# Performance work log

Measured on AMD Instinct MI355X. Metric: run time of the kernel, lower is better.

Reference implementation:

```python
import jax, jax.numpy as jnp
import numpy as np

D = 1  # dilation


def _unfold3x3(x, d):
    # x: [B, C, H, W] -> [B, H*W, 9, C]; matches torch.nn.Unfold(kernel_size=3,
    # dilation=d, padding=d, stride=1) followed by the module's reshapes.
    B, C, H, W = x.shape
    xp = jnp.pad(x, ((0, 0), (0, 0), (d, d), (d, d)))
    pats = [xp[:, :, i * d:i * d + H, j * d:j * d + W] for i in range(3) for j in range(3)]
    p = jnp.stack(pats, axis=0)  # [9, B, C, H, W], kernel positions row-major (center = 4)
    return p.transpose(1, 3, 4, 0, 2).reshape(B, H * W, 9, C)


def _masked_bn(h, m, gamma, beta, eps=1e-5):
    # BatchNorm1d in training mode applied only to rows selected by bool mask m
    # (the torch code gathers rows, BNs them, scatters back into zeros).
    # Stats are the biased mean/var over the selected rows, per channel.
    axes = tuple(range(h.ndim - 1))
    mf = m[..., None].astype(h.dtype)
    n = jnp.maximum(mf.sum(), 1.0)
    mean = (h * mf).sum(axes) / n
    var = (((h - mean) ** 2 * mf)).sum(axes) / n
    return (h - mean) * jax.lax.rsqrt(var + eps) * gamma + beta


def setup_inputs() -> dict:
    key = jax.random.key(0)
    ks = jax.random.split(key, 8)
    B, H, W = 2, 64, 1024
    Cin, Cout, Cm = 64, 64, 4
    s = 0.1
    x = jax.random.normal(ks[0], (B, Cm + Cin, H, W), jnp.float32)
    mask = (jax.random.uniform(ks[1], (B, 1, H, W)) > 0.3).astype(jnp.float32)
    return {
        "x": x,
        "mask": mask,
        "w1": jax.random.normal(ks[2], (8, Cm), jnp.float32) * s,
        "bn1_g": jnp.ones(8, jnp.float32),
        "bn1_b": jnp.zeros(8, jnp.float32),
        "w2": jax.random.normal(ks[3], (1, 8), jnp.float32) * s,
        "b2": jnp.zeros(1, jnp.float32),
        "g1": jax.random.normal(ks[4], (8, Cm), jnp.float32) * s,
        "gbn1_g": jnp.ones(8, jnp.float32),
        "gbn1_b": jnp.zeros(8, jnp.float32),
        "g2": jax.random.normal(ks[5], (8, 8), jnp.float32) * s,
        "gbn2_g": jnp.ones(8, jnp.float32),
        "gbn2_b": jnp.zeros(8, jnp.float32),
        "w_agg": jax.random.normal(ks[6], (Cout, 72 + Cin), jnp.float32) * s,
        "abn_g": jnp.ones(Cout, jnp.float32),
        "abn_b": jnp.zeros(Cout, jnp.float32),
    }


def reference(x, mask, w1, bn1_g, bn1_b, w2, b2, g1, gbn1_g, gbn1_b, g2, gbn2_g, gbn2_b, w_agg, abn_g, abn_b):
    B, C, H, W = x.shape
    xu = _unfold3x3(x, D)                      # [B, HW, 9, C]
    mu = _unfold3x3(mask, D)[..., 0]           # [B, HW, 9]
    msel = mu > 0                              # valid-neighbor mask
    mp0 = msel[:, :, 4]                        # valid-center mask [B, HW]
    pn = xu[..., :4] - xu[:, :, 4:5, :4]       # relative meta coords [B, HW, 9, 4]
    feats = xu[..., 4:]                        # neighbor features [B, HW, 9, Cin]

    # weight branch (dense compute + mask == torch's gather/scatter)
    h = _masked_bn(pn @ w1.T, msel, bn1_g, bn1_b)
    h = jax.nn.relu(h) @ w2.T + b2             # [B, HW, 9, 1]
    wts = jnp.where(msel, h[..., 0], 0.0)      # zeros at invalid neighbors pre-softmax
    wts = jax.nn.softmax(wts, axis=-1)[..., None]

    fagg = (wts * feats).sum(axis=2)           # [B, HW, Cin]

    # geo branch
    g = jax.nn.relu(_masked_bn(pn @ g1.T, msel, gbn1_g, gbn1_b))
    g = jax.nn.relu(_masked_bn(g @ g2.T, msel, gbn2_g, gbn2_b))
    g = jnp.where(msel[..., None], g, 0.0)
    g = (wts * g).reshape(B, H * W, 72)

    # aggregation over valid centers
    out = jnp.concatenate([fagg, g], axis=-1) @ w_agg.T
    out = jax.nn.relu(_masked_bn(out, mp0, abn_g, abn_b))
    out = jnp.where(mp0[..., None], out, 0.0)  # [B, HW, Cout]
    return out.transpose(0, 2, 1).reshape(B, -1, H, W)  # fold with k=1 == reshape
```

## Files before the change

kernel.cpp:

```cpp
#include <hip/hip_runtime.h>

#define HW_ 65536
#define W_ 1024
#define H_ 64
#define B_ 2
#define C_ 68
#define NPIX 131072
#define EPS 1e-5f
#define SCOLS 258
#define STOT (15 * SCOLS)

typedef __attribute__((ext_vector_type(8))) short short8;
typedef __attribute__((ext_vector_type(4))) float floatx4;

__device__ __forceinline__ unsigned short f2bf(float f) {
  unsigned u = __float_as_uint(f);
  u += 0x7fffu + ((u >> 16) & 1u);
  return (unsigned short)(u >> 16);
}
__device__ __forceinline__ unsigned pack2(float a, float b) {
  return (unsigned)f2bf(a) | ((unsigned)f2bf(b) << 16);
}
__device__ __forceinline__ float wred(float v) {
  v += __shfl_xor(v, 1);  v += __shfl_xor(v, 2);  v += __shfl_xor(v, 4);
  v += __shfl_xor(v, 8);  v += __shfl_xor(v, 16); v += __shfl_xor(v, 32);
  return v;
}
__device__ __forceinline__ int swz_tile(int bid) {
  return (bid & 7) * 64 + (bid >> 3);
}

#define XSTG(ch, row, col) stg[((ch) * 3 + (row)) * SCOLS + (col)]
#define MSTG(row, col)     stg[(12 + (row)) * SCOLS + (col)]

template <int NT>
__device__ __forceinline__ void stage_rows(const float* xb, const float* mb,
                                           int h, int w0, float* stg, int tid) {
#pragma unroll 1
  for (int i = tid; i < STOT; i += NT) {
    int seg = i / SCOLS, col = i - seg * SCOLS;
    int arr = seg / 3, row = seg - arr * 3;
    int wg = w0 - 1 + col, hg = h + row - 1;
    bool ok = ((unsigned)wg < (unsigned)W_) && ((unsigned)hg < (unsigned)H_);
    float v = 0.f;
    if (ok) v = (arr < 4) ? xb[(size_t)arr * HW_ + (hg << 10) + wg]
                          : mb[(hg << 10) + wg];
    stg[i] = v;
  }
}

__global__ __launch_bounds__(256, 4) void k_stats1(
    const float* __restrict__ x, const float* __restrict__ mask,
    float* __restrict__ ws) {
  __shared__ float stg[STOT];
  __shared__ float red[4][16];
  int tile = swz_tile(blockIdx.x);
  int p0 = tile * 256;
  int b = p0 >> 16, s0 = p0 & (HW_ - 1);
  int h = s0 >> 10, w0 = s0 & (W_ - 1);
  const float* xb = x + (size_t)b * C_ * HW_;
  const float* mb = mask + (size_t)b * HW_;
  stage_rows<256>(xb, mb, h, w0, stg, threadIdx.x);
  __syncthreads();

  int pix = threadIdx.x;
  float xc0 = XSTG(0, 1, 1 + pix), xc1 = XSTG(1, 1, 1 + pix);
  float xc2 = XSTG(2, 1, 1 + pix), xc3 = XSTG(3, 1, 1 + pix);

  float a[16];
#pragma unroll
  for (int i = 0; i < 16; i++) a[i] = 0.f;
  a[15] = (MSTG(1, 1 + pix) > 0.f) ? 1.f : 0.f;

#pragma unroll
  for (int k = 0; k < 9; k++) {
    int row = k / 3, col = 1 + pix + (k % 3 - 1);
    float mval = MSTG(row, col);
    if (mval > 0.f) {
      float pn0 = XSTG(0, row, col) - xc0;
      float pn1 = XSTG(1, row, col) - xc1;
      float pn2 = XSTG(2, row, col) - xc2;
      float pn3 = XSTG(3, row, col) - xc3;
      a[14] += 1.f;
      a[0] += pn0; a[1] += pn1; a[2] += pn2; a[3] += pn3;
      a[4] += pn0 * pn0; a[5] += pn0 * pn1; a[6] += pn0 * pn2; a[7] += pn0 * pn3;
      a[8] += pn1 * pn1; a[9] += pn1 * pn2; a[10] += pn1 * pn3;
      a[11] += pn2 * pn2; a[12] += pn2 * pn3; a[13] += pn3 * pn3;
    }
  }
  int lane = threadIdx.x & 63, wave = threadIdx.x >> 6;
#pragma unroll
  for (int i = 0; i < 16; i++) {
    float rv = wred(a[i]);
    if (lane == 0) red[wave][i] = rv;
  }
  __syncthreads();
  if (threadIdx.x < 16)
    atomicAdd(&ws[threadIdx.x],
              red[0][threadIdx.x] + red[1][threadIdx.x] + red[2][threadIdx.x] + red[3][threadIdx.x]);
}

__global__ __launch_bounds__(256, 4) void k_stats2(
    const float* __restrict__ x, const float* __restrict__ mask,
    const float* __restrict__ g1, const float* __restrict__ gbn1_g,
    const float* __restrict__ gbn1_b, const float* __restrict__ g2,
    float* __restrict__ ws) {
  __shared__ float stg[STOT];
  __shared__ float red[4][16];
  __shared__ float sc[8], sh[8];
  if (threadIdx.x < 8) {
    int o = threadIdx.x;
    float a0 = g1[o * 4], a1 = g1[o * 4 + 1], a2 = g1[o * 4 + 2], a3 = g1[o * 4 + 3];
    float n = fmaxf(ws[14], 1.f);
    float mean = (a0 * ws[0] + a1 * ws[1] + a2 * ws[2] + a3 * ws[3]) / n;
    float q = a0 * a0 * ws[4] + a1 * a1 * ws[8] + a2 * a2 * ws[11] + a3 * a3 * ws[13]
            + 2.f * (a0 * a1 * ws[5] + a0 * a2 * ws[6] + a0 * a3 * ws[7]
                   + a1 * a2 * ws[9] + a1 * a3 * ws[10] + a2 * a3 * ws[12]);
    float var = q / n - mean * mean;
    float s_ = gbn1_g[o] * rsqrtf(var + EPS);
    sc[o] = s_; sh[o] = gbn1_b[o] - mean * s_;
  }
  int half = blockIdx.x >> 9;
  int tile = swz_tile(blockIdx.x & 511);
  int p0 = tile * 256;
  int b = p0 >> 16, s0 = p0 & (HW_ - 1);
  int h = s0 >> 10, w0 = s0 & (W_ - 1);
  const float* xb = x + (size_t)b * C_ * HW_;
  const float* mb = mask + (size_t)b * HW_;
  stage_rows<256>(xb, mb, h, w0, stg, threadIdx.x);
  __syncthreads();

  int pix = threadIdx.x;
  float xc0 = XSTG(0, 1, 1 + pix), xc1 = XSTG(1, 1, 1 + pix);
  float xc2 = XSTG(2, 1, 1 + pix), xc3 = XSTG(3, 1, 1 + pix);

  float acc2[16];
#pragma unroll
  for (int i = 0; i < 16; i++) acc2[i] = 0.f;

  int kb = half ? 5 : 0, ke = half ? 9 : 5;
#pragma unroll
  for (int k = 0; k < 9; k++) {
    if (k < kb || k >= ke) continue;
    int row = k / 3, col = 1 + pix + (k % 3 - 1);
    float mval = MSTG(row, col);
    if (mval > 0.f) {
      float pn0 = XSTG(0, row, col) - xc0;
      float pn1 = XSTG(1, row, col) - xc1;
      float pn2 = XSTG(2, row, col) - xc2;
      float pn3 = XSTG(3, row, col) - xc3;
      float gb[8];
#pragma unroll
      for (int o = 0; o < 8; o++) {
        float tg = pn0 * g1[o * 4] + pn1 * g1[o * 4 + 1] + pn2 * g1[o * 4 + 2] + pn3 * g1[o * 4 + 3];
        gb[o] = fmaxf(sc[o] * tg + sh[o], 0.f);
      }
#pragma unroll
      for (int j = 0; j < 8; j++) {
        float t2 = 0.f;
#pragma unroll
        for (int o = 0; o < 8; o++) t2 += gb[o] * g2[j * 8 + o];
        acc2[j] += t2; acc2[8 + j] += t2 * t2;
      }
    }
  }
  int lane = threadIdx.x & 63, wave = threadIdx.x >> 6;
#pragma unroll
  for (int i = 0; i < 16; i++) {
    float rv = wred(acc2[i]);
    if (lane == 0) red[wave][i] = rv;
  }
  __syncthreads();
  if (threadIdx.x < 16)
    atomicAdd(&ws[40 + threadIdx.x],
              red[0][threadIdx.x] + red[1][threadIdx.x] + red[2][threadIdx.x] + red[3][threadIdx.x]);
}

__global__ __launch_bounds__(512, 4) void k_fused(
    const float* __restrict__ x, const float* __restrict__ mask,
    const float* __restrict__ w1, const float* __restrict__ bn1_g,
    const float* __restrict__ bn1_b, const float* __restrict__ w2,
    const float* __restrict__ b2, const float* __restrict__ g1,
    const float* __restrict__ gbn1_g, const float* __restrict__ gbn1_b,
    const float* __restrict__ g2, const float* __restrict__ gbn2_g,
    const float* __restrict__ gbn2_b, const float* __restrict__ w_agg,
    const float* __restrict__ ws, float* __restrict__ out_pre,
    float* __restrict__ wsum) {
  __shared__ uint4 vecA[17][256];
  __shared__ float evb[9][256];
  __shared__ float sA[8], hA[8], sG1[8], hG1[8], sG2[8], hG2[8];
  float* stg = (float*)&vecA[0][0];

  if (threadIdx.x < 16) {
    int o = threadIdx.x & 7;
    const float* wv = (threadIdx.x < 8) ? w1 : g1;
    float a0 = wv[o * 4], a1 = wv[o * 4 + 1], a2 = wv[o * 4 + 2], a3 = wv[o * 4 + 3];
    float n = fmaxf(ws[14], 1.f);
    float mean = (a0 * ws[0] + a1 * ws[1] + a2 * ws[2] + a3 * ws[3]) / n;
    float q = a0 * a0 * ws[4] + a1 * a1 * ws[8] + a2 * a2 * ws[11] + a3 * a3 * ws[13]
            + 2.f * (a0 * a1 * ws[5] + a0 * a2 * ws[6] + a0 * a3 * ws[7]
                   + a1 * a2 * ws[9] + a1 * a3 * ws[10] + a2 * a3 * ws[12]);
    float var = q / n - mean * mean;
    float gma = (threadIdx.x < 8) ? bn1_g[o] : gbn1_g[o];
    float bta = (threadIdx.x < 8) ? bn1_b[o] : gbn1_b[o];
    float s_ = gma * rsqrtf(var + EPS);
    float sft = bta - mean * s_;
    if (threadIdx.x < 8) { sA[o] = s_;  hA[o] = sft; }
    else                 { sG1[o] = s_; hG1[o] = sft; }
  } else if (threadIdx.x < 24) {
    int o = threadIdx.x & 7;
    float n = fmaxf(ws[14], 1.f);
    float mean = ws[40 + o] / n, var = ws[48 + o] / n - mean * mean;
    float s_ = gbn2_g[o] * rsqrtf(var + EPS);
    sG2[o] = s_; hG2[o] = gbn2_b[o] - mean * s_;
  }

  int tid = threadIdx.x;
  int half = tid >> 8;
  int pix = tid & 255;
  int tile = swz_tile(blockIdx.x);
  int p0 = tile * 256;
  int b = p0 >> 16, s0 = p0 & (HW_ - 1);
  int h = s0 >> 10, w0 = s0 & (W_ - 1);
  const float* xb = x + (size_t)b * C_ * HW_;
  const float* mb = mask + (size_t)b * HW_;
  stage_rows<512>(xb, mb, h, w0, stg, tid);
  __syncthreads();

  float xc0 = XSTG(0, 1, 1 + pix), xc1 = XSTG(1, 1, 1 + pix);
  float xc2 = XSTG(2, 1, 1 + pix), xc3 = XSTG(3, 1, 1 + pix);
  float b2v = b2[0];

  float pnc[5][4];
  unsigned mbits = 0u;
  int kb = half ? 5 : 0, ke = half ? 9 : 5;
#pragma unroll
  for (int k = 0; k < 9; k++) {
    if (k < kb || k >= ke) continue;
    int j = k - kb;
    int row = k / 3, col = 1 + pix + (k % 3 - 1);
    float mval = MSTG(row, col);
    float wp = 0.f;
    pnc[j][0] = 0.f; pnc[j][1] = 0.f; pnc[j][2] = 0.f; pnc[j][3] = 0.f;
    if (mval > 0.f) {
      mbits |= (1u << k);
      pnc[j][0] = XSTG(0, row, col) - xc0;
      pnc[j][1] = XSTG(1, row, col) - xc1;
      pnc[j][2] = XSTG(2, row, col) - xc2;
      pnc[j][3] = XSTG(3, row, col) - xc3;
      float accw = 0.f;
#pragma unroll
      for (int o = 0; o < 8; o++) {
        float ta = pnc[j][0] * w1[o * 4] + pnc[j][1] * w1[o * 4 + 1] +
                   pnc[j][2] * w1[o * 4 + 2] + pnc[j][3] * w1[o * 4 + 3];
        accw += fmaxf(sA[o] * ta + hA[o], 0.f) * w2[o];
      }
      wp = accw + b2v;
    }
    evb[k][pix] = wp;
  }
  __syncthreads();

  float ev[9];
  float mx = -1e30f;
#pragma unroll
  for (int k = 0; k < 9; k++) { ev[k] = evb[k][pix]; mx = fmaxf(mx, ev[k]); }
  float den = 0.f;
#pragma unroll
  for (int k = 0; k < 9; k++) { ev[k] = __expf(ev[k] - mx); den += ev[k]; }
  float inv = 1.f / den;

#pragma unroll
  for (int k = 0; k < 9; k++) {
    if (k < kb || k >= ke) continue;
    int j = k - kb;
    uint4 pk; pk.x = pk.y = pk.z = pk.w = 0u;
    if ((mbits >> k) & 1u) {
      float wt = ev[k] * inv;
      float gb[8];
#pragma unroll
      for (int o = 0; o < 8; o++) {
        float tg = pnc[j][0] * g1[o * 4] + pnc[j][1] * g1[o * 4 + 1] +
                   pnc[j][2] * g1[o * 4 + 2] + pnc[j][3] * g1[o * 4 + 3];
        gb[o] = fmaxf(sG1[o] * tg + hG1[o], 0.f);
      }
      float gv[8];
#pragma unroll
      for (int j2 = 0; j2 < 8; j2++) {
        float t2 = 0.f;
#pragma unroll
        for (int o = 0; o < 8; o++) t2 += gb[o] * g2[j2 * 8 + o];
        float gg = fmaxf(sG2[j2] * t2 + hG2[j2], 0.f);
        gv[j2] = wt * gg;
      }
      pk.x = pack2(gv[0], gv[1]); pk.y = pack2(gv[2], gv[3]);
      pk.z = pack2(gv[4], gv[5]); pk.w = pack2(gv[6], gv[7]);
    }
    vecA[8 + k][pix] = pk;
  }

  float facc[32];
#pragma unroll
  for (int c = 0; c < 32; c++) facc[c] = 0.f;
#pragma unroll
  for (int k = 0; k < 9; k++) {
    int di = k / 3 - 1, dj = k % 3 - 1;
    int hh = h + di, ww = w0 + pix + dj;
    bool inb = ((unsigned)hh < (unsigned)H_) && ((unsigned)ww < (unsigned)W_);
    if (inb) {
      int ns = (hh << 10) + ww;
      float wt = ev[k] * inv;
      const float* xf = xb + (size_t)(4 + half * 32) * HW_ + ns;
#pragma unroll
      for (int c = 0; c < 32; c++) facc[c] += wt * xf[(size_t)c * HW_];
    }
  }
#pragma unroll
  for (int c0 = 0; c0 < 32; c0 += 8) {
    uint4 pk;
    pk.x = pack2(facc[c0], facc[c0 + 1]);     pk.y = pack2(facc[c0 + 2], facc[c0 + 3]);
    pk.z = pack2(facc[c0 + 4], facc[c0 + 5]); pk.w = pack2(facc[c0 + 6], facc[c0 + 7]);
    vecA[(half * 32 + c0) >> 3][pix] = pk;
  }
  __syncthreads();

  int lane = tid & 63, wave = tid >> 6;
  int q = lane >> 4, r = lane & 15;
  int wr = wave >> 1, wc = wave & 1;

  short8 Bf[2][5];
#pragma unroll
  for (int nt = 0; nt < 2; nt++) {
    int n = wc * 32 + nt * 16 + r;
#pragma unroll
    for (int ks = 0; ks < 5; ks++) {
      int k0 = ks * 32 + q * 8;
      uint4 pk; pk.x = pk.y = pk.z = pk.w = 0u;
      if (k0 < 136) {
        float4 f0 = *reinterpret_cast<const float4*>(w_agg + n * 136 + k0);
        float4 f1 = *reinterpret_cast<const float4*>(w_agg + n * 136 + k0 + 4);
        pk.x = pack2(f0.x, f0.y); pk.y = pack2(f0.z, f0.w);
        pk.z = pack2(f1.x, f1.y); pk.w = pack2(f1.z, f1.w);
      }
      Bf[nt][ks] = *reinterpret_cast<short8*>(&pk);
    }
  }

  floatx4 acc[4][2];
#pragma unroll
  for (int m = 0; m < 4; m++)
#pragma unroll
    for (int nt = 0; nt < 2; nt++) acc[m][nt] = (floatx4){0.f, 0.f, 0.f, 0.f};

#pragma unroll
  for (int m = 0; m < 4; m++) {
    int pixm = (wr * 4 + m) * 16 + r;
    short8 Af[5];
#pragma unroll
    for (int ks = 0; ks < 5; ks++) {
      int chunk = ks * 4 + q;
      if (chunk < 17)
        Af[ks] = *reinterpret_cast<const short8*>(&vecA[chunk][pixm]);
      else
        Af[ks] = (short8){0, 0, 0, 0, 0, 0, 0, 0};
    }
#pragma unroll
    for (int nt = 0; nt < 2; nt++)
#pragma unroll
      for (int ks = 0; ks < 5; ks++)
        acc[m][nt] = __builtin_amdgcn_mfma_f32_16x16x32_bf16(Af[ks], Bf[nt][ks], acc[m][nt], 0, 0, 0);
  }

  float aS[2] = {0.f, 0.f}, aQ[2] = {0.f, 0.f};
#pragma unroll
  for (int m = 0; m < 4; m++) {
    int mt = wr * 4 + m;
    int srow = s0 + mt * 16 + q * 4;
    float4 mv = *reinterpret_cast<const float4*>(mb + srow);
    float m0 = (mv.x > 0.f) ? 1.f : 0.f, m1 = (mv.y > 0.f) ? 1.f : 0.f;
    float m2 = (mv.z > 0.f) ? 1.f : 0.f, m3 = (mv.w > 0.f) ? 1.f : 0.f;
#pragma unroll
    for (int nt = 0; nt < 2; nt++) {
      int ch = wc * 32 + nt * 16 + r;
      float4 ov;
      ov.x = acc[m][nt][0]; ov.y = acc[m][nt][1];
      ov.z = acc[m][nt][2]; ov.w = acc[m][nt][3];
      aS[nt] += ov.x * m0 + ov.y * m1 + ov.z * m2 + ov.w * m3;
      aQ[nt] += ov.x * ov.x * m0 + ov.y * ov.y * m1 + ov.z * ov.z * m2 + ov.w * ov.w * m3;
      *reinterpret_cast<float4*>(out_pre + ((size_t)(b * 64 + ch)) * HW_ + srow) = ov;
    }
  }

  __syncthreads();
  float* rS = (float*)&vecA[0][0];
  float* rQ = rS + 256;
#pragma unroll
  for (int nt = 0; nt < 2; nt++) {
    float v1 = aS[nt], v2 = aQ[nt];
    v1 += __shfl_xor(v1, 16); v1 += __shfl_xor(v1, 32);
    v2 += __shfl_xor(v2, 16); v2 += __shfl_xor(v2, 32);
    if (lane < 16) { rS[wave * 32 + nt * 16 + lane] = v1; rQ[wave * 32 + nt * 16 + lane] = v2; }
  }
  __syncthreads();
  if (tid < 64) {
    int c = tid;
    int wc_ = c >> 5, nt_ = (c >> 4) & 1, r_ = c & 15;
    float s1 = 0.f, s2 = 0.f;
#pragma unroll
    for (int wr_ = 0; wr_ < 4; wr_++) {
      int idx = (wr_ * 2 + wc_) * 32 + nt_ * 16 + r_;
      s1 += rS[idx]; s2 += rQ[idx];
    }
    atomicAdd(&wsum[64 + c], s1);
    atomicAdd(&wsum[128 + c], s2);
  }
}

__global__ __launch_bounds__(256) void k_final(
    const float* __restrict__ out_pre, const float* __restrict__ mask,
    const float* __restrict__ abn_g, const float* __restrict__ abn_b,
    const float* __restrict__ ws, float* __restrict__ out) {
  __shared__ float sc[64], sh[64];
  if (threadIdx.x < 64) {
    int c = threadIdx.x;
    float n0 = fmaxf(ws[15], 1.f);
    float mean = ws[64 + c] / n0;
    float var = ws[128 + c] / n0 - mean * mean;
    float s_ = abn_g[c] * rsqrtf(var + EPS);
    sc[c] = s_; sh[c] = abn_b[c] - mean * s_;
  }
  __syncthreads();
  int i4 = (blockIdx.x * 256 + threadIdx.x) * 4;
  if (i4 >= B_ * 64 * HW_) return;
  int c = (i4 >> 16) & 63;
  int b = i4 >> 22;
  int s = i4 & (HW_ - 1);
  float4 v = *reinterpret_cast<const float4*>(out_pre + i4);
  float4 m = *reinterpret_cast<const float4*>(mask + (size_t)b * HW_ + s);
  float4 o;
  o.x = (m.x > 0.f) ? fmaxf(v.x * sc[c] + sh[c], 0.f) : 0.f;
  o.y = (m.y > 0.f) ? fmaxf(v.y * sc[c] + sh[c], 0.f) : 0.f;
  o.z = (m.z > 0.f) ? fmaxf(v.z * sc[c] + sh[c], 0.f) : 0.f;
  o.w = (m.w > 0.f) ? fmaxf(v.w * sc[c] + sh[c], 0.f) : 0.f;
  *reinterpret_cast<float4*>(out + i4) = o;
}

extern "C" void kernel_launch(void* const* d_in, const int* in_sizes, int n_in,
                              void* d_out, int out_size, void* d_ws, size_t ws_size,
                              hipStream_t stream) {
  const float* x      = (const float*)d_in[0];
  const float* mask   = (const float*)d_in[1];
  const float* w1     = (const float*)d_in[2];
  const float* bn1_g  = (const float*)d_in[3];
  const float* bn1_b  = (const float*)d_in[4];
  const float* w2     = (const float*)d_in[5];
  const float* b2     = (const float*)d_in[6];
  const float* g1     = (const float*)d_in[7];
  const float* gbn1_g = (const float*)d_in[8];
  const float* gbn1_b = (const float*)d_in[9];
  const float* g2     = (const float*)d_in[10];
  const float* gbn2_g = (const float*)d_in[11];
  const float* gbn2_b = (const float*)d_in[12];
  const float* w_agg  = (const float*)d_in[13];
  const float* abn_g  = (const float*)d_in[14];
  const float* abn_b  = (const float*)d_in[15];
  float* out = (float*)d_out;

  size_t need = 1024 + (size_t)NPIX * 64 * 4;
  if (ws_size < need) return;

  float* wsf = (float*)d_ws;
  float* out_pre = (float*)((char*)d_ws + 1024);

  hipMemsetAsync(d_ws, 0, 1024, stream);
  k_stats1<<<512, 256, 0, stream>>>(x, mask, wsf);
  k_stats2<<<1024, 256, 0, stream>>>(x, mask, g1, gbn1_g, gbn1_b, g2, wsf);
  k_fused<<<512, 512, 0, stream>>>(x, mask, w1, bn1_g, bn1_b, w2, b2, g1,
                                   gbn1_g, gbn1_b, g2, gbn2_g, gbn2_b, w_agg,
                                   wsf, out_pre, wsf);
  k_final<<<8192, 256, 0, stream>>>(out_pre, mask, abn_g, abn_b, wsf, out);
}
```

Before: 194.0 us.

## Split fused kernel into 128-pixel tiles with four thread quarters per pixel

The fused kernel now handles 128 pixels per block instead of 256 and launches twice as many blocks. Each pixel's work is split across four thread quarters rather than two: each quarter covers a subset of the 9 neighbors and 16 feature channels. Shared memory shrinks and the occupancy hint rises to 6 blocks, aiming at more parallelism and latency hiding. The cost is more redundant staging halo loads and per-block setup, plus smaller MFMA tiles per wave.

```diff
diff --git a/kernel.cpp b/kernel.cpp
--- a/kernel.cpp
+++ b/kernel.cpp
@@ -8,7 +8,7 @@
 #define NPIX 131072
 #define EPS 1e-5f
 #define SCOLS 258
-#define STOT (15 * SCOLS)
+#define FSC 130
 
 typedef __attribute__((ext_vector_type(8))) short short8;
 typedef __attribute__((ext_vector_type(4))) float floatx4;
@@ -30,15 +30,13 @@
   return (bid & 7) * 64 + (bid >> 3);
 }
 
-#define XSTG(ch, row, col) stg[((ch) * 3 + (row)) * SCOLS + (col)]
-#define MSTG(row, col)     stg[(12 + (row)) * SCOLS + (col)]
-
-template <int NT>
+template <int NT, int SC>
 __device__ __forceinline__ void stage_rows(const float* xb, const float* mb,
                                            int h, int w0, float* stg, int tid) {
+  const int tot = 15 * SC;
 #pragma unroll 1
-  for (int i = tid; i < STOT; i += NT) {
-    int seg = i / SCOLS, col = i - seg * SCOLS;
+  for (int i = tid; i < tot; i += NT) {
+    int seg = i / SC, col = i - seg * SC;
     int arr = seg / 3, row = seg - arr * 3;
     int wg = w0 - 1 + col, hg = h + row - 1;
     bool ok = ((unsigned)wg < (unsigned)W_) && ((unsigned)hg < (unsigned)H_);
@@ -49,10 +47,15 @@
   }
 }
 
+#define XSTG(ch, row, col) stg[((ch) * 3 + (row)) * SCOLS + (col)]
+#define MSTG(row, col)     stg[(12 + (row)) * SCOLS + (col)]
+#define XF(ch, row, col)   stg[((ch) * 3 + (row)) * FSC + (col)]
+#define MF(row, col)       stg[(12 + (row)) * FSC + (col)]
+
 __global__ __launch_bounds__(256, 4) void k_stats1(
     const float* __restrict__ x, const float* __restrict__ mask,
     float* __restrict__ ws) {
-  __shared__ float stg[STOT];
+  __shared__ float stg[15 * SCOLS];
   __shared__ float red[4][16];
   int tile = swz_tile(blockIdx.x);
   int p0 = tile * 256;
@@ -60,7 +63,7 @@
   int h = s0 >> 10, w0 = s0 & (W_ - 1);
   const float* xb = x + (size_t)b * C_ * HW_;
   const float* mb = mask + (size_t)b * HW_;
-  stage_rows<256>(xb, mb, h, w0, stg, threadIdx.x);
+  stage_rows<256, SCOLS>(xb, mb, h, w0, stg, threadIdx.x);
   __syncthreads();
 
   int pix = threadIdx.x;
@@ -105,7 +108,7 @@
     const float* __restrict__ g1, const float* __restrict__ gbn1_g,
     const float* __restrict__ gbn1_b, const float* __restrict__ g2,
     float* __restrict__ ws) {
-  __shared__ float stg[STOT];
+  __shared__ float stg[15 * SCOLS];
   __shared__ float red[4][16];
   __shared__ float sc[8], sh[8];
   if (threadIdx.x < 8) {
@@ -127,7 +130,7 @@
   int h = s0 >> 10, w0 = s0 & (W_ - 1);
   const float* xb = x + (size_t)b * C_ * HW_;
   const float* mb = mask + (size_t)b * HW_;
-  stage_rows<256>(xb, mb, h, w0, stg, threadIdx.x);
+  stage_rows<256, SCOLS>(xb, mb, h, w0, stg, threadIdx.x);
   __syncthreads();
 
   int pix = threadIdx.x;
@@ -176,7 +179,7 @@
               red[0][threadIdx.x] + red[1][threadIdx.x] + red[2][threadIdx.x] + red[3][threadIdx.x]);
 }
 
-__global__ __launch_bounds__(512, 4) void k_fused(
+__global__ __launch_bounds__(512, 6) void k_fused(
     const float* __restrict__ x, const float* __restrict__ mask,
     const float* __restrict__ w1, const float* __restrict__ bn1_g,
     const float* __restrict__ bn1_b, const float* __restrict__ w2,
@@ -186,8 +189,8 @@
     const float* __restrict__ gbn2_b, const float* __restrict__ w_agg,
     const float* __restrict__ ws, float* __restrict__ out_pre,
     float* __restrict__ wsum) {
-  __shared__ uint4 vecA[17][256];
-  __shared__ float evb[9][256];
+  __shared__ uint4 vecA[17][128];
+  __shared__ float evb[9][128];
   __shared__ float sA[8], hA[8], sG1[8], hG1[8], sG2[8], hG2[8];
   float* stg = (float*)&vecA[0][0];
 
@@ -216,38 +219,40 @@
   }
 
   int tid = threadIdx.x;
-  int half = tid >> 8;
-  int pix = tid & 255;
-  int tile = swz_tile(blockIdx.x);
-  int p0 = tile * 256;
+  int quarter = tid >> 7;
+  int pix = tid & 127;
+  int tile = (blockIdx.x & 7) * 128 + (blockIdx.x >> 3);
+  int p0 = tile * 128;
   int b = p0 >> 16, s0 = p0 & (HW_ - 1);
   int h = s0 >> 10, w0 = s0 & (W_ - 1);
   const float* xb = x + (size_t)b * C_ * HW_;
   const float* mb = mask + (size_t)b * HW_;
-  stage_rows<512>(xb, mb, h, w0, stg, tid);
-  __syncthreads();
-
-  float xc0 = XSTG(0, 1, 1 + pix), xc1 = XSTG(1, 1, 1 + pix);
-  float xc2 = XSTG(2, 1, 1 + pix), xc3 = XSTG(3, 1, 1 + pix);
+  stage_rows<512, FSC>(xb, mb, h, w0, stg, tid);
+  __syncthreads();
+
+  float xc0 = XF(0, 1, 1 + pix), xc1 = XF(1, 1, 1 + pix);
+  float xc2 = XF(2, 1, 1 + pix), xc3 = XF(3, 1, 1 + pix);
   float b2v = b2[0];
 
-  float pnc[5][4];
+  int kb = (quarter == 0) ? 0 : (2 * quarter + 1);
+  int ke = 2 * quarter + 3;
+
+  float pnc[3][4];
   unsigned mbits = 0u;
-  int kb = half ? 5 : 0, ke = half ? 9 : 5;
 #pragma unroll
   for (int k = 0; k < 9; k++) {
     if (k < kb || k >= ke) continue;
     int j = k - kb;
     int row = k / 3, col = 1 + pix + (k % 3 - 1);
-    float mval = MSTG(row, col);
+    float mval = MF(row, col);
     float wp = 0.f;
     pnc[j][0] = 0.f; pnc[j][1] = 0.f; pnc[j][2] = 0.f; pnc[j][3] = 0.f;
     if (mval > 0.f) {
       mbits |= (1u << k);
-      pnc[j][0] = XSTG(0, row, col) - xc0;
-      pnc[j][1] = XSTG(1, row, col) - xc1;
-      pnc[j][2] = XSTG(2, row, col) - xc2;
-      pnc[j][3] = XSTG(3, row, col) - xc3;
+      pnc[j][0] = XF(0, row, col) - xc0;
+      pnc[j][1] = XF(1, row, col) - xc1;
+      pnc[j][2] = XF(2, row, col) - xc2;
+      pnc[j][3] = XF(3, row, col) - xc3;
       float accw = 0.f;
 #pragma unroll
       for (int o = 0; o < 8; o++) {
@@ -299,9 +304,9 @@
     vecA[8 + k][pix] = pk;
   }
 
-  float facc[32];
-#pragma unroll
-  for (int c = 0; c < 32; c++) facc[c] = 0.f;
+  float facc[16];
+#pragma unroll
+  for (int c = 0; c < 16; c++) facc[c] = 0.f;
 #pragma unroll
   for (int k = 0; k < 9; k++) {
     int di = k / 3 - 1, dj = k % 3 - 1;
@@ -310,17 +315,17 @@
     if (inb) {
       int ns = (hh << 10) + ww;
       float wt = ev[k] * inv;
-      const float* xf = xb + (size_t)(4 + half * 32) * HW_ + ns;
-#pragma unroll
-      for (int c = 0; c < 32; c++) facc[c] += wt * xf[(size_t)c * HW_];
-    }
-  }
-#pragma unroll
-  for (int c0 = 0; c0 < 32; c0 += 8) {
+      const float* xf = xb + (size_t)(4 + quarter * 16) * HW_ + ns;
+#pragma unroll
+      for (int c = 0; c < 16; c++) facc[c] += wt * xf[(size_t)c * HW_];
+    }
+  }
+#pragma unroll
+  for (int c0 = 0; c0 < 16; c0 += 8) {
     uint4 pk;
     pk.x = pack2(facc[c0], facc[c0 + 1]);     pk.y = pack2(facc[c0 + 2], facc[c0 + 3]);
     pk.z = pack2(facc[c0 + 4], facc[c0 + 5]); pk.w = pack2(facc[c0 + 6], facc[c0 + 7]);
-    vecA[(half * 32 + c0) >> 3][pix] = pk;
+    vecA[quarter * 2 + (c0 >> 3)][pix] = pk;
   }
   __syncthreads();
 
@@ -346,15 +351,15 @@
     }
   }
 
-  floatx4 acc[4][2];
-#pragma unroll
-  for (int m = 0; m < 4; m++)
+  floatx4 acc[2][2];
+#pragma unroll
+  for (int m = 0; m < 2; m++)
 #pragma unroll
     for (int nt = 0; nt < 2; nt++) acc[m][nt] = (floatx4){0.f, 0.f, 0.f, 0.f};
 
 #pragma unroll
-  for (int m = 0; m < 4; m++) {
-    int pixm = (wr * 4 + m) * 16 + r;
+  for (int m = 0; m < 2; m++) {
+    int pixm = (wr * 2 + m) * 16 + r;
     short8 Af[5];
 #pragma unroll
     for (int ks = 0; ks < 5; ks++) {
@@ -373,8 +378,8 @@
 
   float aS[2] = {0.f, 0.f}, aQ[2] = {0.f, 0.f};
 #pragma unroll
-  for (int m = 0; m < 4; m++) {
-    int mt = wr * 4 + m;
+  for (int m = 0; m < 2; m++) {
+    int mt = wr * 2 + m;
     int srow = s0 + mt * 16 + q * 4;
     float4 mv = *reinterpret_cast<const float4*>(mb + srow);
     float m0 = (mv.x > 0.f) ? 1.f : 0.f, m1 = (mv.y > 0.f) ? 1.f : 0.f;
@@ -475,8 +480,8 @@
   hipMemsetAsync(d_ws, 0, 1024, stream);
   k_stats1<<<512, 256, 0, stream>>>(x, mask, wsf);
   k_stats2<<<1024, 256, 0, stream>>>(x, mask, g1, gbn1_g, gbn1_b, g2, wsf);
-  k_fused<<<512, 512, 0, stream>>>(x, mask, w1, bn1_g, bn1_b, w2, b2, g1,
-                                   gbn1_g, gbn1_b, g2, gbn2_g, gbn2_b, w_agg,
-                                   wsf, out_pre, wsf);
+  k_fused<<<1024, 512, 0, stream>>>(x, mask, w1, bn1_g, bn1_b, w2, b2, g1,
+                                    gbn1_g, gbn1_b, g2, gbn2_g, gbn2_b, w_agg,
+                                    wsf, out_pre, wsf);
   k_final<<<8192, 256, 0, stream>>>(out_pre, mask, abn_g, abn_b, wsf, out);
 }
```

Result: slower. 240.1 us (+23.7%).

## Drop memset, replace stats1 atomics with per-block partials, pre-convert w_agg to bf16

Applied to the files above, without the earlier changes.

Removes the hipMemsetAsync launch: k_stats1 now zeroes the remaining accumulator slots itself and writes per-block partial moments to the workspace instead of issuing atomics. k_stats2 reduces those 512 partials in every block before computing the BN scale and shift. k_stats1 also converts w_agg to bf16 once into the workspace, so k_fused loads packed bf16 directly instead of converting floats in each block. The cost is a redundant reduction of 512x16 floats in each of the 1024 k_stats2 blocks and a larger workspace requirement.

```diff
diff --git a/kernel.cpp b/kernel.cpp
--- a/kernel.cpp
+++ b/kernel.cpp
@@ -8,7 +8,6 @@
 #define NPIX 131072
 #define EPS 1e-5f
 #define SCOLS 258
-#define STOT (15 * SCOLS)
 
 typedef __attribute__((ext_vector_type(8))) short short8;
 typedef __attribute__((ext_vector_type(4))) float floatx4;
@@ -30,14 +29,13 @@
   return (bid & 7) * 64 + (bid >> 3);
 }
 
-#define XSTG(ch, row, col) stg[((ch) * 3 + (row)) * SCOLS + (col)]
-#define MSTG(row, col)     stg[(12 + (row)) * SCOLS + (col)]
 
 template <int NT>
 __device__ __forceinline__ void stage_rows(const float* xb, const float* mb,
                                            int h, int w0, float* stg, int tid) {
+  const int tot = 15 * SCOLS;
 #pragma unroll 1
-  for (int i = tid; i < STOT; i += NT) {
+  for (int i = tid; i < tot; i += NT) {
     int seg = i / SCOLS, col = i - seg * SCOLS;
     int arr = seg / 3, row = seg - arr * 3;
     int wg = w0 - 1 + col, hg = h + row - 1;
@@ -49,11 +47,21 @@
   }
 }
 
+#define XSTG(ch, row, col) stg[((ch) * 3 + (row)) * SCOLS + (col)]
+#define MSTG(row, col)     stg[(12 + (row)) * SCOLS + (col)]
+
 __global__ __launch_bounds__(256, 4) void k_stats1(
     const float* __restrict__ x, const float* __restrict__ mask,
-    float* __restrict__ ws) {
-  __shared__ float stg[STOT];
+    const float* __restrict__ w_agg, float* __restrict__ ws) {
+  __shared__ float stg[15 * SCOLS];
   __shared__ float red[4][16];
+
+  if (blockIdx.x == 0 && threadIdx.x < 240) ws[16 + threadIdx.x] = 0.f;
+  if (blockIdx.x < 64 && threadIdx.x < 136) {
+    unsigned short* wb = (unsigned short*)((char*)ws + 40960);
+    wb[blockIdx.x * 136 + threadIdx.x] = f2bf(w_agg[blockIdx.x * 136 + threadIdx.x]);
+  }
+
   int tile = swz_tile(blockIdx.x);
   int p0 = tile * 256;
   int b = p0 >> 16, s0 = p0 & (HW_ - 1);
@@ -96,8 +104,8 @@
   }
   __syncthreads();
   if (threadIdx.x < 16)
-    atomicAdd(&ws[threadIdx.x],
-              red[0][threadIdx.x] + red[1][threadIdx.x] + red[2][threadIdx.x] + red[3][threadIdx.x]);
+    ws[256 + blockIdx.x * 16 + threadIdx.x] =
+        red[0][threadIdx.x] + red[1][threadIdx.x] + red[2][threadIdx.x] + red[3][threadIdx.x];
 }
 
 __global__ __launch_bounds__(256, 4) void k_stats2(
@@ -105,21 +113,42 @@
     const float* __restrict__ g1, const float* __restrict__ gbn1_g,
     const float* __restrict__ gbn1_b, const float* __restrict__ g2,
     float* __restrict__ ws) {
-  __shared__ float stg[STOT];
+  __shared__ float stg[15 * SCOLS];
   __shared__ float red[4][16];
+  __shared__ float red2[16][17];
+  __shared__ float smom[16];
   __shared__ float sc[8], sh[8];
+
+  {
+    int i = threadIdx.x & 15, bg = threadIdx.x >> 4;
+    const float* pb = ws + 256 + bg * 32 * 16;
+    float s = 0.f;
+#pragma unroll 8
+    for (int bb = 0; bb < 32; bb++) s += pb[bb * 16 + i];
+    red2[bg][i] = s;
+  }
+  __syncthreads();
+  if (threadIdx.x < 16) {
+    float s = 0.f;
+#pragma unroll
+    for (int g = 0; g < 16; g++) s += red2[g][threadIdx.x];
+    smom[threadIdx.x] = s;
+    ws[threadIdx.x] = s;
+  }
+  __syncthreads();
   if (threadIdx.x < 8) {
     int o = threadIdx.x;
     float a0 = g1[o * 4], a1 = g1[o * 4 + 1], a2 = g1[o * 4 + 2], a3 = g1[o * 4 + 3];
-    float n = fmaxf(ws[14], 1.f);
-    float mean = (a0 * ws[0] + a1 * ws[1] + a2 * ws[2] + a3 * ws[3]) / n;
-    float q = a0 * a0 * ws[4] + a1 * a1 * ws[8] + a2 * a2 * ws[11] + a3 * a3 * ws[13]
-            + 2.f * (a0 * a1 * ws[5] + a0 * a2 * ws[6] + a0 * a3 * ws[7]
-                   + a1 * a2 * ws[9] + a1 * a3 * ws[10] + a2 * a3 * ws[12]);
+    float n = fmaxf(smom[14], 1.f);
+    float mean = (a0 * smom[0] + a1 * smom[1] + a2 * smom[2] + a3 * smom[3]) / n;
+    float q = a0 * a0 * smom[4] + a1 * a1 * smom[8] + a2 * a2 * smom[11] + a3 * a3 * smom[13]
+            + 2.f * (a0 * a1 * smom[5] + a0 * a2 * smom[6] + a0 * a3 * smom[7]
+                   + a1 * a2 * smom[9] + a1 * a3 * smom[10] + a2 * a3 * smom[12]);
     float var = q / n - mean * mean;
     float s_ = gbn1_g[o] * rsqrtf(var + EPS);
     sc[o] = s_; sh[o] = gbn1_b[o] - mean * s_;
   }
+
   int half = blockIdx.x >> 9;
   int tile = swz_tile(blockIdx.x & 511);
   int p0 = tile * 256;
@@ -183,7 +212,7 @@
     const float* __restrict__ b2, const float* __restrict__ g1,
     const float* __restrict__ gbn1_g, const float* __restrict__ gbn1_b,
     const float* __restrict__ g2, const float* __restrict__ gbn2_g,
-    const float* __restrict__ gbn2_b, const float* __restrict__ w_agg,
+    const float* __restrict__ gbn2_b, const unsigned short* __restrict__ wb,
     const float* __restrict__ ws, float* __restrict__ out_pre,
     float* __restrict__ wsum) {
   __shared__ uint4 vecA[17][256];
@@ -336,12 +365,8 @@
     for (int ks = 0; ks < 5; ks++) {
       int k0 = ks * 32 + q * 8;
       uint4 pk; pk.x = pk.y = pk.z = pk.w = 0u;
-      if (k0 < 136) {
-        float4 f0 = *reinterpret_cast<const float4*>(w_agg + n * 136 + k0);
-        float4 f1 = *reinterpret_cast<const float4*>(w_agg + n * 136 + k0 + 4);
-        pk.x = pack2(f0.x, f0.y); pk.y = pack2(f0.z, f0.w);
-        pk.z = pack2(f1.x, f1.y); pk.w = pack2(f1.z, f1.w);
-      }
+      if (k0 < 136)
+        pk = *reinterpret_cast<const uint4*>(wb + n * 136 + k0);
       Bf[nt][ks] = *reinterpret_cast<short8*>(&pk);
     }
   }
@@ -466,17 +491,17 @@
   const float* abn_b  = (const float*)d_in[15];
   float* out = (float*)d_out;
 
-  size_t need = 1024 + (size_t)NPIX * 64 * 4;
+  size_t need = 65536 + (size_t)NPIX * 64 * 4;
   if (ws_size < need) return;
 
   float* wsf = (float*)d_ws;
-  float* out_pre = (float*)((char*)d_ws + 1024);
-
-  hipMemsetAsync(d_ws, 0, 1024, stream);
-  k_stats1<<<512, 256, 0, stream>>>(x, mask, wsf);
+  const unsigned short* wb = (const unsigned short*)((char*)d_ws + 40960);
+  float* out_pre = (float*)((char*)d_ws + 65536);
+
+  k_stats1<<<512, 256, 0, stream>>>(x, mask, w_agg, wsf);
   k_stats2<<<1024, 256, 0, stream>>>(x, mask, g1, gbn1_g, gbn1_b, g2, wsf);
   k_fused<<<512, 512, 0, stream>>>(x, mask, w1, bn1_g, bn1_b, w2, b2, g1,
-                                   gbn1_g, gbn1_b, g2, gbn2_g, gbn2_b, w_agg,
+                                   gbn1_g, gbn1_b, g2, gbn2_g, gbn2_b, wb,
                                    wsf, out_pre, wsf);
   k_final<<<8192, 256, 0, stream>>>(out_pre, mask, abn_g, abn_b, wsf, out);
 }
```

After: 185.6 us (median of 2 runs). 4.4% less time.
